# Kernel tuning notes

Measured on AMD Instinct MI355X. Metric: run time of the kernel, lower is better.

## Reference

```python
import jax, jax.numpy as jnp
import numpy as np

N, E, C = 50000, 800000, 100000
D_IN, HID = 128, 128
MLP_IN, MLP_HID = 2 * HID + 1, HID // 2
BN_EPS = 1e-5
NEG_SLOPE = 0.01


def setup_inputs() -> dict:
    key = jax.random.key(0)
    ks = jax.random.split(key, 24)
    inp = {
        "x": jax.random.normal(ks[0], (N, D_IN), jnp.float32),
        "src": jax.random.randint(ks[1], (E,), 0, N, jnp.int32),
        "dst": jax.random.randint(ks[2], (E,), 0, N, jnp.int32),
        "cand_u": jax.random.randint(ks[3], (C,), 0, N, jnp.int32),
        "cand_v": jax.random.randint(ks[4], (C,), 0, N, jnp.int32),
        "cand_feat": jax.random.normal(ks[5], (C, 1), jnp.float32),
    }
    s = 1.0 / np.sqrt(D_IN)
    # SAGEConv layer 0 and 1 (in=out=128 since statedim == pnhid)
    for li, k0 in [(0, 6), (1, 12)]:
        inp[f"w_self{li}"] = jax.random.uniform(ks[k0], (D_IN, HID), jnp.float32, -s, s)
        inp[f"w_neigh{li}"] = jax.random.uniform(ks[k0 + 1], (D_IN, HID), jnp.float32, -s, s)
        inp[f"b{li}"] = jnp.zeros((HID,), jnp.float32)
        inp[f"gamma{li}"] = jnp.ones((HID,), jnp.float32)
        inp[f"beta{li}"] = jnp.zeros((HID,), jnp.float32)
        inp[f"rm{li}"] = jax.random.normal(ks[k0 + 2], (HID,), jnp.float32) * 0.1
        inp[f"rv{li}"] = jax.random.uniform(ks[k0 + 3], (HID,), jnp.float32, 0.5, 1.5)
    # confidence MLP: 257 -> 64 -> 64 -> 1
    sizes = [MLP_IN, MLP_HID, MLP_HID, 1]
    for i in range(3):
        si = 1.0 / np.sqrt(sizes[i])
        inp[f"mw{i}"] = jax.random.uniform(ks[18 + 2 * i], (sizes[i], sizes[i + 1]), jnp.float32, -si, si)
        inp[f"mb{i}"] = jax.random.uniform(ks[19 + 2 * i], (sizes[i + 1],), jnp.float32, -si, si)
    return inp


def _sage_bn_block(x, src, dst, w_self, w_neigh, b, gamma, beta, rm, rv):
    # mean aggregation over incoming edges (gather -> scatter-add -> divide)
    msgs = x[src]  # [E, D]
    agg = jax.ops.segment_sum(msgs, dst, num_segments=N)  # [N, D]
    deg = jax.ops.segment_sum(jnp.ones((src.shape[0],), x.dtype), dst, num_segments=N)
    agg = agg / jnp.maximum(deg, 1.0)[:, None]
    h = x @ w_self + agg @ w_neigh + b
    # BatchNorm1d (eval mode, running stats) then leaky_relu; dropout is identity in eval
    h = gamma * (h - rm) * jax.lax.rsqrt(rv + BN_EPS) + beta
    return jax.nn.leaky_relu(h, NEG_SLOPE)


def reference(x, src, dst, cand_u, cand_v, cand_feat,
              w_self0, w_neigh0, b0, gamma0, beta0, rm0, rv0,
              w_self1, w_neigh1, b1, gamma1, beta1, rm1, rv1,
              mw0, mb0, mw1, mb1, mw2, mb2):
    h = _sage_bn_block(x, src, dst, w_self0, w_neigh0, b0, gamma0, beta0, rm0, rv0)
    h = _sage_bn_block(h, src, dst, w_self1, w_neigh1, b1, gamma1, beta1, rm1, rv1)
    h = jnp.nan_to_num(h, nan=1e-14)
    # candidate embeddings: [C, 2*HID + 1]
    ce = jnp.concatenate([h[cand_u], h[cand_v], cand_feat], axis=-1)
    z = jax.nn.leaky_relu(ce @ mw0 + mb0, NEG_SLOPE)
    z = jax.nn.leaky_relu(z @ mw1 + mb1, NEG_SLOPE)
    y = z @ mw2 + mb2  # [C, 1]
    return y, jax.nn.softmax(y, axis=0)
```

## Files before the change

kernel.cpp:

```cpp
#include <hip/hip_runtime.h>
#include <math.h>

#define N_NODES 50000
#define N_EDGES 800000
#define N_CAND  100000
#define D       128
#define BN_EPS  1e-5f
#define SLOPE   0.01f

#define NB2     196
#define TILE    4096
#define NTILE   196
#define BCAP    4736

typedef __attribute__((ext_vector_type(8))) short bf16x8;
typedef __attribute__((ext_vector_type(4))) float f32x4;

__device__ __forceinline__ float lrelu(float x){ return x >= 0.f ? x : SLOPE * x; }

__device__ __forceinline__ unsigned short f2bf_rn(float f){
  unsigned int u = __float_as_uint(f);
  unsigned int r = u + 0x7FFFu + ((u >> 16) & 1u);
  return (unsigned short)(r >> 16);
}
__device__ __forceinline__ float bf2f(unsigned short h){
  return __uint_as_float(((unsigned int)h) << 16);
}
__device__ __forceinline__ float bfu(unsigned u){ return __uint_as_float(u << 16); }
__device__ __forceinline__ float bfh(unsigned u){ return __uint_as_float(u & 0xffff0000u); }
__device__ __forceinline__ float4 bf4f(ushort4 u){
  return make_float4(__uint_as_float((unsigned)u.x << 16),
                     __uint_as_float((unsigned)u.y << 16),
                     __uint_as_float((unsigned)u.z << 16),
                     __uint_as_float((unsigned)u.w << 16));
}

__device__ __forceinline__ unsigned pk_bf16(float a, float b){
  unsigned r;
  asm("v_cvt_pk_bf16_f32 %0, %1, %2" : "=v"(r) : "v"(a), "v"(b));
  return r;
}
__device__ __forceinline__ void split2(float a, float b, unsigned &h, unsigned &l){
  h = pk_bf16(a, b);
  float ra = a - __uint_as_float(h << 16);
  float rb = b - __uint_as_float(h & 0xffff0000u);
  l = pk_bf16(ra, rb);
}

__global__ __launch_bounds__(256) void k_bin(const int* __restrict__ src, const int* __restrict__ dst,
                                             int* __restrict__ gcnt, unsigned* __restrict__ ebin, int E){
  __shared__ unsigned stage[TILE];
  __shared__ int hist[256], lscan[256], lex[256], lcur[256], gbase[256];
  __shared__ int stot;
  int t = threadIdx.x;
  int e0 = blockIdx.x * TILE;

  hist[t] = 0;
  __syncthreads();

  unsigned pk[16]; int bk[16]; bool ok[16];
  #pragma unroll
  for (int j = 0; j < 16; ++j){
    int i = e0 + j * 256 + t;
    ok[j] = (i < E);
    if (ok[j]){
      int d = dst[i];
      pk[j] = ((unsigned)d << 16) | (unsigned)src[i];
      bk[j] = d >> 8;
      atomicAdd(&hist[bk[j]], 1);
    }
  }
  __syncthreads();

  lscan[t] = hist[t];
  __syncthreads();
  for (int off = 1; off < 256; off <<= 1){
    int v = (t >= off) ? lscan[t - off] : 0;
    __syncthreads();
    lscan[t] += v;
    __syncthreads();
  }
  int ex = lscan[t] - hist[t];
  lex[t]  = ex;
  lcur[t] = ex;
  if (t < NB2) gbase[t] = hist[t] ? atomicAdd(&gcnt[t], hist[t]) : 0;
  if (t == 255) stot = lscan[255];
  __syncthreads();

  #pragma unroll
  for (int j = 0; j < 16; ++j){
    if (ok[j]){
      int p = atomicAdd(&lcur[bk[j]], 1);
      stage[p] = pk[j];
    }
  }
  __syncthreads();

  int tot = stot;
  for (int i = t; i < tot; i += 256){
    unsigned e = stage[i];
    int b = (int)(e >> 24);
    ebin[(size_t)b * BCAP + gbase[b] + (i - lex[b])] = e;
  }
}

__global__ __launch_bounds__(256) void k_bscan2(const int* __restrict__ gcnt, int* __restrict__ bbase,
                                                int* __restrict__ rowptr){
  __shared__ int sd[256];
  int t = threadIdx.x;
  int v = (t < NB2) ? gcnt[t] : 0;
  sd[t] = v; __syncthreads();
  for (int off = 1; off < 256; off <<= 1){
    int a = (t >= off) ? sd[t - off] : 0;
    __syncthreads();
    sd[t] += a; __syncthreads();
  }
  if (t < NB2) bbase[t] = sd[t] - v;
  if (t == NB2 - 1) rowptr[N_NODES] = sd[t];
}

__global__ __launch_bounds__(256) void k_bfin(const int* __restrict__ gcnt, const int* __restrict__ bbase,
                                              const unsigned* __restrict__ ebin,
                                              unsigned short* __restrict__ eid16,
                                              int* __restrict__ rowptr, int n){
  __shared__ int hist[256], lb[256], lcur[256];
  int t = threadIdx.x, b = blockIdx.x;
  int cb   = gcnt[b];
  int base = bbase[b];
  const unsigned* eb = &ebin[(size_t)b * BCAP];
  hist[t] = 0;
  __syncthreads();
  for (int idx = t; idx < cb; idx += 256) atomicAdd(&hist[(eb[idx] >> 16) & 255], 1);
  __syncthreads();
  lb[t] = hist[t];
  __syncthreads();
  for (int off = 1; off < 256; off <<= 1){
    int v = (t >= off) ? lb[t - off] : 0;
    __syncthreads();
    lb[t] += v; __syncthreads();
  }
  int ex = lb[t] - hist[t];
  lcur[t] = ex;
  int node = (b << 8) + t;
  if (node < n) rowptr[node] = base + ex;
  __syncthreads();
  for (int idx = t; idx < cb; idx += 256){
    unsigned e = eb[idx];
    int p = atomicAdd(&lcur[(e >> 16) & 255], 1);
    eid16[base + p] = (unsigned short)(e & 0xffffu);
  }
}

__global__ __launch_bounds__(256) void k_cvt_w(const float* __restrict__ ws, const float* __restrict__ wn,
                                               unsigned short* __restrict__ bth, unsigned short* __restrict__ btl){
  int col = blockIdx.x;
  int k   = threadIdx.x;
  float v = (k < 128) ? ws[k * D + col] : wn[(k - 128) * D + col];
  unsigned short hi = f2bf_rn(v);
  unsigned short lo = f2bf_rn(v - bf2f(hi));
  bth[col * 256 + k] = hi;
  btl[col * 256 + k] = lo;
}

__global__ __launch_bounds__(256) void k_cvt_mlp(const float* __restrict__ w, int K, int Kpad,
                                                 unsigned short* __restrict__ th, unsigned short* __restrict__ tl){
  int col = blockIdx.x;
  for (int k = threadIdx.x; k < Kpad; k += 256){
    float v = (k < K) ? w[k * 64 + col] : 0.f;
    unsigned short hi = f2bf_rn(v);
    th[col * Kpad + k] = hi;
    tl[col * Kpad + k] = f2bf_rn(v - bf2f(hi));
  }
}

__global__ __launch_bounds__(128) void k_cvt_w0cat(const float* __restrict__ mw0,
                                                   unsigned short* __restrict__ ch, unsigned short* __restrict__ cl_){
  int col = blockIdx.x;
  int k   = threadIdx.x;
  float v = (col < 64) ? mw0[k * 64 + col] : mw0[(128 + k) * 64 + (col - 64)];
  unsigned short hi = f2bf_rn(v);
  ch [col * 128 + k] = hi;
  cl_[col * 128 + k] = f2bf_rn(v - bf2f(hi));
}

__global__ __launch_bounds__(256) void k_cvt_x(const float* __restrict__ X, unsigned short* __restrict__ XB, int nel4){
  int i = blockIdx.x * 256 + threadIdx.x;
  if (i < nel4){
    float4 v = *reinterpret_cast<const float4*>(&X[(size_t)i * 4]);
    ushort4 u;
    u.x = f2bf_rn(v.x); u.y = f2bf_rn(v.y); u.z = f2bf_rn(v.z); u.w = f2bf_rn(v.w);
    *reinterpret_cast<ushort4*>(&XB[(size_t)i * 4]) = u;
  }
}

__global__ __launch_bounds__(256) void k_agg_bf(const unsigned short* __restrict__ XB,
                                                const int* __restrict__ rowptr, const unsigned short* __restrict__ eid,
                                                float* __restrict__ AG, int n){
  int g = blockIdx.x * 8 + (threadIdx.x >> 5);
  int l = threadIdx.x & 31;
  if (g >= n) return;
  int e0 = rowptr[g], e1 = rowptr[g + 1];
  float4 a0 = make_float4(0.f,0.f,0.f,0.f);
  float4 a1 = make_float4(0.f,0.f,0.f,0.f);
  float4 a2 = make_float4(0.f,0.f,0.f,0.f);
  float4 a3 = make_float4(0.f,0.f,0.f,0.f);
  int e = e0;
  for (; e + 4 <= e1; e += 4){
    int s0 = eid[e], s1 = eid[e + 1], s2 = eid[e + 2], s3 = eid[e + 3];
    ushort4 u0 = *reinterpret_cast<const ushort4*>(&XB[(size_t)s0 * D + l * 4]);
    ushort4 u1 = *reinterpret_cast<const ushort4*>(&XB[(size_t)s1 * D + l * 4]);
    ushort4 u2 = *reinterpret_cast<const ushort4*>(&XB[(size_t)s2 * D + l * 4]);
    ushort4 u3 = *reinterpret_cast<const ushort4*>(&XB[(size_t)s3 * D + l * 4]);
    float4 f0 = bf4f(u0), f1 = bf4f(u1), f2 = bf4f(u2), f3 = bf4f(u3);
    a0.x += f0.x; a0.y += f0.y; a0.z += f0.z; a0.w += f0.w;
    a1.x += f1.x; a1.y += f1.y; a1.z += f1.z; a1.w += f1.w;
    a2.x += f2.x; a2.y += f2.y; a2.z += f2.z; a2.w += f2.w;
    a3.x += f3.x; a3.y += f3.y; a3.z += f3.z; a3.w += f3.w;
  }
  for (; e < e1; ++e){
    int s0 = eid[e];
    ushort4 u0 = *reinterpret_cast<const ushort4*>(&XB[(size_t)s0 * D + l * 4]);
    float4 f0 = bf4f(u0);
    a0.x += f0.x; a0.y += f0.y; a0.z += f0.z; a0.w += f0.w;
  }
  float sc = 1.f / fmaxf((float)(e1 - e0), 1.f);
  float4 o;
  o.x = (a0.x + a1.x + a2.x + a3.x) * sc;
  o.y = (a0.y + a1.y + a2.y + a3.y) * sc;
  o.z = (a0.z + a1.z + a2.z + a3.z) * sc;
  o.w = (a0.w + a1.w + a2.w + a3.w) * sc;
  *reinterpret_cast<float4*>(&AG[(size_t)g * D + l * 4]) = o;
}

__global__ __launch_bounds__(256) void k_sage_mfma(const float* __restrict__ XS, const float* __restrict__ AG,
    const unsigned short* __restrict__ BTH, const unsigned short* __restrict__ BTL,
    const float* __restrict__ Bb, const float* __restrict__ GM, const float* __restrict__ BT,
    const float* __restrict__ RM, const float* __restrict__ RV,
    float* __restrict__ H, unsigned short* __restrict__ HBH, unsigned short* __restrict__ HBL,
    int n, int donan)
{
  __shared__ unsigned short Ah[64 * 40];
  __shared__ unsigned short Al[64 * 40];
  __shared__ unsigned short Bh[128 * 40];
  __shared__ unsigned short Bl[128 * 40];

  int t  = threadIdx.x;
  int l  = t & 63;
  int wv = t >> 6;
  int lm = l & 15;
  int lk = l >> 4;
  int node0 = blockIdx.x * 64;

  f32x4 acc[8];
  #pragma unroll
  for (int f = 0; f < 8; ++f) acc[f] = (f32x4){0.f, 0.f, 0.f, 0.f};

  for (int step = 0; step < 8; ++step){
    int k0 = step * 32;
    const float* srcA = (step < 4) ? XS : AG;
    int koff = (step < 4) ? k0 : (k0 - 128);

    __syncthreads();
    #pragma unroll
    for (int i = 0; i < 2; ++i){
      int c   = t + i * 256;
      int row = c >> 3, c4 = c & 7;
      int node = min(node0 + row, n - 1);
      float4 v = *reinterpret_cast<const float4*>(&srcA[(size_t)node * D + koff + c4 * 4]);
      const float* vp = (const float*)&v;
      unsigned short hh[4], ll[4];
      #pragma unroll
      for (int j = 0; j < 4; ++j){
        unsigned short hi = f2bf_rn(vp[j]);
        hh[j] = hi;
        ll[j] = f2bf_rn(vp[j] - bf2f(hi));
      }
      uint2 wh, wl;
      wh.x = (unsigned)hh[0] | ((unsigned)hh[1] << 16);
      wh.y = (unsigned)hh[2] | ((unsigned)hh[3] << 16);
      wl.x = (unsigned)ll[0] | ((unsigned)ll[1] << 16);
      wl.y = (unsigned)ll[2] | ((unsigned)ll[3] << 16);
      *reinterpret_cast<uint2*>(&Ah[row * 40 + c4 * 4]) = wh;
      *reinterpret_cast<uint2*>(&Al[row * 40 + c4 * 4]) = wl;
    }
    #pragma unroll
    for (int i = 0; i < 2; ++i){
      int c   = t + i * 256;
      int col = c >> 2, q = c & 3;
      *reinterpret_cast<uint4*>(&Bh[col * 40 + q * 8]) =
          *reinterpret_cast<const uint4*>(&BTH[col * 256 + k0 + q * 8]);
      *reinterpret_cast<uint4*>(&Bl[col * 40 + q * 8]) =
          *reinterpret_cast<const uint4*>(&BTL[col * 256 + k0 + q * 8]);
    }
    __syncthreads();

    bf16x8 afh = *reinterpret_cast<const bf16x8*>(&Ah[(wv * 16 + lm) * 40 + lk * 8]);
    bf16x8 afl = *reinterpret_cast<const bf16x8*>(&Al[(wv * 16 + lm) * 40 + lk * 8]);
    #pragma unroll
    for (int f = 0; f < 8; ++f){
      bf16x8 bfh = *reinterpret_cast<const bf16x8*>(&Bh[(f * 16 + lm) * 40 + lk * 8]);
      bf16x8 bfl = *reinterpret_cast<const bf16x8*>(&Bl[(f * 16 + lm) * 40 + lk * 8]);
      acc[f] = __builtin_amdgcn_mfma_f32_16x16x32_bf16(afh, bfh, acc[f], 0, 0, 0);
      acc[f] = __builtin_amdgcn_mfma_f32_16x16x32_bf16(afl, bfh, acc[f], 0, 0, 0);
      acc[f] = __builtin_amdgcn_mfma_f32_16x16x32_bf16(afh, bfl, acc[f], 0, 0, 0);
    }
  }

  #pragma unroll
  for (int f = 0; f < 8; ++f){
    int col = f * 16 + lm;
    float s  = GM[col] * rsqrtf(RV[col] + BN_EPS);
    float cj = (Bb[col] - RM[col]) * s + BT[col];
    #pragma unroll
    for (int r = 0; r < 4; ++r){
      int node = node0 + wv * 16 + lk * 4 + r;
      if (node < n){
        float v = lrelu(acc[f][r] * s + cj);
        if (donan && (v != v)) v = 1e-14f;
        if (H)  H[(size_t)node * D + col] = v;
        unsigned short h16 = f2bf_rn(v);
        if (HBH) HBH[(size_t)node * D + col] = h16;
        if (HBL) HBL[(size_t)node * D + col] = f2bf_rn(v - bf2f(h16));
      }
    }
  }
}

__global__ __launch_bounds__(256) void k_pgemm(
    const unsigned short* __restrict__ HH, const unsigned short* __restrict__ HL,
    const unsigned short* __restrict__ WCH, const unsigned short* __restrict__ WCL,
    unsigned short* __restrict__ PH, unsigned short* __restrict__ PL, int n)
{
  __shared__ unsigned short Ah[64 * 40];
  __shared__ unsigned short Al[64 * 40];
  __shared__ unsigned short Bh[128 * 40];
  __shared__ unsigned short Bl[128 * 40];

  int t  = threadIdx.x;
  int l  = t & 63;
  int wv = t >> 6;
  int lm = l & 15;
  int lk = l >> 4;
  int node0 = blockIdx.x * 64;

  f32x4 acc[8];
  #pragma unroll
  for (int f = 0; f < 8; ++f) acc[f] = (f32x4){0.f, 0.f, 0.f, 0.f};

  for (int step = 0; step < 4; ++step){
    int k0 = step * 32;
    __syncthreads();
    {
      int row = t >> 2, q = t & 3;
      int node = min(node0 + row, n - 1);
      *reinterpret_cast<uint4*>(&Ah[row * 40 + q * 8]) =
          *reinterpret_cast<const uint4*>(&HH[(size_t)node * D + k0 + q * 8]);
      *reinterpret_cast<uint4*>(&Al[row * 40 + q * 8]) =
          *reinterpret_cast<const uint4*>(&HL[(size_t)node * D + k0 + q * 8]);
    }
    #pragma unroll
    for (int i = 0; i < 2; ++i){
      int c = t + i * 256;
      int col = c >> 2, q = c & 3;
      *reinterpret_cast<uint4*>(&Bh[col * 40 + q * 8]) =
          *reinterpret_cast<const uint4*>(&WCH[col * 128 + k0 + q * 8]);
      *reinterpret_cast<uint4*>(&Bl[col * 40 + q * 8]) =
          *reinterpret_cast<const uint4*>(&WCL[col * 128 + k0 + q * 8]);
    }
    __syncthreads();

    bf16x8 afh = *reinterpret_cast<const bf16x8*>(&Ah[(wv * 16 + lm) * 40 + lk * 8]);
    bf16x8 afl = *reinterpret_cast<const bf16x8*>(&Al[(wv * 16 + lm) * 40 + lk * 8]);
    #pragma unroll
    for (int f = 0; f < 8; ++f){
      bf16x8 bfh = *reinterpret_cast<const bf16x8*>(&Bh[(f * 16 + lm) * 40 + lk * 8]);
      bf16x8 bfl = *reinterpret_cast<const bf16x8*>(&Bl[(f * 16 + lm) * 40 + lk * 8]);
      acc[f] = __builtin_amdgcn_mfma_f32_16x16x32_bf16(afh, bfh, acc[f], 0, 0, 0);
      acc[f] = __builtin_amdgcn_mfma_f32_16x16x32_bf16(afl, bfh, acc[f], 0, 0, 0);
      acc[f] = __builtin_amdgcn_mfma_f32_16x16x32_bf16(afh, bfl, acc[f], 0, 0, 0);
    }
  }

  #pragma unroll
  for (int f = 0; f < 8; ++f){
    int col = f * 16 + lm;
    #pragma unroll
    for (int r = 0; r < 4; ++r){
      int node = node0 + wv * 16 + lk * 4 + r;
      if (node < n){
        float v = acc[f][r];
        unsigned short h16 = f2bf_rn(v);
        PH[(size_t)node * D + col] = h16;
        PL[(size_t)node * D + col] = f2bf_rn(v - bf2f(h16));
      }
    }
  }
}

__device__ __forceinline__ void proc2(unsigned uh, unsigned ul, unsigned vh, unsigned vl,
                                      float wfa, float wfb, float b0a, float b0b, float cfv,
                                      unsigned &ho, unsigned &lo_){
  float z0 = lrelu(bfu(uh) + bfu(ul) + bfu(vh) + bfu(vl) + cfv * wfa + b0a);
  float z1 = lrelu(bfh(uh) + bfh(ul) + bfh(vh) + bfh(vl) + cfv * wfb + b0b);
  split2(z0, z1, ho, lo_);
}

__global__ __launch_bounds__(256) void k_mlp2(
    const unsigned short* __restrict__ PH, const unsigned short* __restrict__ PL,
    const int* __restrict__ cu, const int* __restrict__ cv, const float* __restrict__ cf,
    const float* __restrict__ mw0, const float* __restrict__ mb0,
    const unsigned short* __restrict__ W1H, const unsigned short* __restrict__ W1L,
    const float* __restrict__ mb1, const float* __restrict__ mw2, const float* __restrict__ mb2,
    float* __restrict__ y, int C)
{
  __shared__ unsigned short zh[4][32 * 72];
  __shared__ unsigned short zl[4][32 * 72];
  __shared__ float bw[64], ww[64];

  int t = threadIdx.x;
  int wv = t >> 6, l = t & 63, lm = l & 15, lk = l >> 4;
  int cl = l & 31, hsel = l >> 5;
  int candbase = blockIdx.x * 128 + wv * 32;

  if (t < 64){ bw[t] = mb0[t]; ww[t] = mw0[256 * 64 + t]; }
  __syncthreads();

  int cc = min(candbase + cl, C - 1);
  int nu = cu[cc], nv = cv[cc];
  float cfv = cf[cc];

  const uint4* puh = reinterpret_cast<const uint4*>(&PH[(size_t)nu * D + hsel * 32]);
  const uint4* pul = reinterpret_cast<const uint4*>(&PL[(size_t)nu * D + hsel * 32]);
  const uint4* pvh = reinterpret_cast<const uint4*>(&PH[(size_t)nv * D + 64 + hsel * 32]);
  const uint4* pvl = reinterpret_cast<const uint4*>(&PL[(size_t)nv * D + 64 + hsel * 32]);
  uint4 uh0 = puh[0], uh1 = puh[1], uh2 = puh[2], uh3 = puh[3];
  uint4 ul0 = pul[0], ul1 = pul[1], ul2 = pul[2], ul3 = pul[3];
  uint4 vh0 = pvh[0], vh1 = pvh[1], vh2 = pvh[2], vh3 = pvh[3];
  uint4 vl0 = pvl[0], vl1 = pvl[1], vl2 = pvl[2], vl3 = pvl[3];

  int colb = hsel * 32;
  unsigned short* zhr = &zh[wv][cl * 72];
  unsigned short* zlr = &zl[wv][cl * 72];
  #define PROC_W(UH, UL, VH, VL, CO) { \
    unsigned ho, lo_; \
    proc2(UH, UL, VH, VL, ww[colb + (CO)], ww[colb + (CO) + 1], bw[colb + (CO)], bw[colb + (CO) + 1], cfv, ho, lo_); \
    *reinterpret_cast<unsigned*>(&zhr[colb + (CO)]) = ho; \
    *reinterpret_cast<unsigned*>(&zlr[colb + (CO)]) = lo_; }
  PROC_W(uh0.x, ul0.x, vh0.x, vl0.x, 0)  PROC_W(uh0.y, ul0.y, vh0.y, vl0.y, 2)
  PROC_W(uh0.z, ul0.z, vh0.z, vl0.z, 4)  PROC_W(uh0.w, ul0.w, vh0.w, vl0.w, 6)
  PROC_W(uh1.x, ul1.x, vh1.x, vl1.x, 8)  PROC_W(uh1.y, ul1.y, vh1.y, vl1.y, 10)
  PROC_W(uh1.z, ul1.z, vh1.z, vl1.z, 12) PROC_W(uh1.w, ul1.w, vh1.w, vl1.w, 14)
  PROC_W(uh2.x, ul2.x, vh2.x, vl2.x, 16) PROC_W(uh2.y, ul2.y, vh2.y, vl2.y, 18)
  PROC_W(uh2.z, ul2.z, vh2.z, vl2.z, 20) PROC_W(uh2.w, ul2.w, vh2.w, vl2.w, 22)
  PROC_W(uh3.x, ul3.x, vh3.x, vl3.x, 24) PROC_W(uh3.y, ul3.y, vh3.y, vl3.y, 26)
  PROC_W(uh3.z, ul3.z, vh3.z, vl3.z, 28) PROC_W(uh3.w, ul3.w, vh3.w, vl3.w, 30)
  #undef PROC_W

  int kbase = lk * 8;
  f32x4 a2[2][4];
  #pragma unroll
  for (int m = 0; m < 2; ++m)
    #pragma unroll
    for (int f = 0; f < 4; ++f) a2[m][f] = (f32x4){0.f, 0.f, 0.f, 0.f};

  #pragma unroll
  for (int s2 = 0; s2 < 2; ++s2){
    int kk = s2 * 32 + kbase;
    bf16x8 azh0 = *reinterpret_cast<const bf16x8*>(&zh[wv][(0 * 16 + lm) * 72 + kk]);
    bf16x8 azl0 = *reinterpret_cast<const bf16x8*>(&zl[wv][(0 * 16 + lm) * 72 + kk]);
    bf16x8 azh1 = *reinterpret_cast<const bf16x8*>(&zh[wv][(1 * 16 + lm) * 72 + kk]);
    bf16x8 azl1 = *reinterpret_cast<const bf16x8*>(&zl[wv][(1 * 16 + lm) * 72 + kk]);
    #pragma unroll
    for (int f = 0; f < 4; ++f){
      int col = f * 16 + lm;
      bf16x8 bh = *reinterpret_cast<const bf16x8*>(&W1H[(size_t)col * 64 + kk]);
      bf16x8 bl = *reinterpret_cast<const bf16x8*>(&W1L[(size_t)col * 64 + kk]);
      a2[0][f] = __builtin_amdgcn_mfma_f32_16x16x32_bf16(azh0, bh, a2[0][f], 0, 0, 0);
      a2[0][f] = __builtin_amdgcn_mfma_f32_16x16x32_bf16(azl0, bh, a2[0][f], 0, 0, 0);
      a2[0][f] = __builtin_amdgcn_mfma_f32_16x16x32_bf16(azh0, bl, a2[0][f], 0, 0, 0);
      a2[1][f] = __builtin_amdgcn_mfma_f32_16x16x32_bf16(azh1, bh, a2[1][f], 0, 0, 0);
      a2[1][f] = __builtin_amdgcn_mfma_f32_16x16x32_bf16(azl1, bh, a2[1][f], 0, 0, 0);
      a2[1][f] = __builtin_amdgcn_mfma_f32_16x16x32_bf16(azh1, bl, a2[1][f], 0, 0, 0);
    }
  }

  float p00 = 0.f, p01 = 0.f, p02 = 0.f, p03 = 0.f;
  float p10 = 0.f, p11 = 0.f, p12 = 0.f, p13 = 0.f;
  #pragma unroll
  for (int f = 0; f < 4; ++f){
    int col = f * 16 + lm;
    float b1v = mb1[col];
    float w2v = mw2[col];
    p00 = fmaf(lrelu(a2[0][f][0] + b1v), w2v, p00);
    p01 = fmaf(lrelu(a2[0][f][1] + b1v), w2v, p01);
    p02 = fmaf(lrelu(a2[0][f][2] + b1v), w2v, p02);
    p03 = fmaf(lrelu(a2[0][f][3] + b1v), w2v, p03);
    p10 = fmaf(lrelu(a2[1][f][0] + b1v), w2v, p10);
    p11 = fmaf(lrelu(a2[1][f][1] + b1v), w2v, p11);
    p12 = fmaf(lrelu(a2[1][f][2] + b1v), w2v, p12);
    p13 = fmaf(lrelu(a2[1][f][3] + b1v), w2v, p13);
  }
  #pragma unroll
  for (int off = 1; off < 16; off <<= 1){
    p00 += __shfl_xor(p00, off); p01 += __shfl_xor(p01, off);
    p02 += __shfl_xor(p02, off); p03 += __shfl_xor(p03, off);
    p10 += __shfl_xor(p10, off); p11 += __shfl_xor(p11, off);
    p12 += __shfl_xor(p12, off); p13 += __shfl_xor(p13, off);
  }
  if (lm == 0){
    float b2 = mb2[0];
    int base0 = candbase + lk * 4;
    int base1 = candbase + 16 + lk * 4;
    if (base0 + 0 < C) y[base0 + 0] = p00 + b2;
    if (base0 + 1 < C) y[base0 + 1] = p01 + b2;
    if (base0 + 2 < C) y[base0 + 2] = p02 + b2;
    if (base0 + 3 < C) y[base0 + 3] = p03 + b2;
    if (base1 + 0 < C) y[base1 + 0] = p10 + b2;
    if (base1 + 1 < C) y[base1 + 1] = p11 + b2;
    if (base1 + 2 < C) y[base1 + 2] = p12 + b2;
    if (base1 + 3 < C) y[base1 + 3] = p13 + b2;
  }
}

__global__ __launch_bounds__(256) void k_red1(const float* __restrict__ y,
                                              float* __restrict__ bmax, float* __restrict__ bsum, int C){
  __shared__ float sm[4];
  __shared__ float ss[4];
  int t = threadIdx.x;
  float m = -3.4e38f;
  for (int i = blockIdx.x * 256 + t; i < C; i += gridDim.x * 256) m = fmaxf(m, y[i]);
  for (int o = 32; o; o >>= 1) m = fmaxf(m, __shfl_xor(m, o));
  if ((t & 63) == 0) sm[t >> 6] = m;
  __syncthreads();
  float bm = fmaxf(fmaxf(sm[0], sm[1]), fmaxf(sm[2], sm[3]));
  float s = 0.f;
  for (int i = blockIdx.x * 256 + t; i < C; i += gridDim.x * 256) s += expf(y[i] - bm);
  for (int o = 32; o; o >>= 1) s += __shfl_xor(s, o);
  if ((t & 63) == 0) ss[t >> 6] = s;
  __syncthreads();
  if (t == 0){ bmax[blockIdx.x] = bm; bsum[blockIdx.x] = ss[0] + ss[1] + ss[2] + ss[3]; }
}

__global__ __launch_bounds__(256) void k_red2(const float* __restrict__ bmax, const float* __restrict__ bsum,
                                              float* __restrict__ g, int nb){
  __shared__ float sm[4];
  __shared__ float ss[4];
  int t = threadIdx.x;
  float m0 = (t < nb) ? bmax[t] : -3.4e38f;
  float m = m0;
  for (int o = 32; o; o >>= 1) m = fmaxf(m, __shfl_xor(m, o));
  if ((t & 63) == 0) sm[t >> 6] = m;
  __syncthreads();
  float gm = fmaxf(fmaxf(sm[0], sm[1]), fmaxf(sm[2], sm[3]));
  float s = (t < nb) ? bsum[t] * expf(m0 - gm) : 0.f;
  for (int o = 32; o; o >>= 1) s += __shfl_xor(s, o);
  if ((t & 63) == 0) ss[t >> 6] = s;
  __syncthreads();
  if (t == 0){ g[0] = gm; g[1] = 1.f / (ss[0] + ss[1] + ss[2] + ss[3]); }
}

__global__ __launch_bounds__(256) void k_red3(const float* __restrict__ y, const float* __restrict__ g,
                                              float* __restrict__ out, int C){
  int i = blockIdx.x * 256 + threadIdx.x;
  if (i < C) out[i] = expf(y[i] - g[0]) * g[1];
}

extern "C" void kernel_launch(void* const* d_in, const int* in_sizes, int n_in,
                              void* d_out, int out_size, void* d_ws, size_t ws_size,
                              hipStream_t stream)
{
  const float* x   = (const float*)d_in[0];
  const int*   src = (const int*)  d_in[1];
  const int*   dst = (const int*)  d_in[2];
  const int*   cu  = (const int*)  d_in[3];
  const int*   cv  = (const int*)  d_in[4];
  const float* cf  = (const float*)d_in[5];
  const float* ws0 = (const float*)d_in[6];
  const float* wn0 = (const float*)d_in[7];
  const float* b0  = (const float*)d_in[8];
  const float* g0  = (const float*)d_in[9];
  const float* be0 = (const float*)d_in[10];
  const float* rm0 = (const float*)d_in[11];
  const float* rv0 = (const float*)d_in[12];
  const float* ws1 = (const float*)d_in[13];
  const float* wn1 = (const float*)d_in[14];
  const float* b1  = (const float*)d_in[15];
  const float* g1  = (const float*)d_in[16];
  const float* be1 = (const float*)d_in[17];
  const float* rm1 = (const float*)d_in[18];
  const float* rv1 = (const float*)d_in[19];
  const float* mw0 = (const float*)d_in[20];
  const float* mb0 = (const float*)d_in[21];
  const float* mw1 = (const float*)d_in[22];
  const float* mb1 = (const float*)d_in[23];
  const float* mw2 = (const float*)d_in[24];
  const float* mb2 = (const float*)d_in[25];

  float* out = (float*)d_out;

  char* w = (char*)d_ws;
  float* aggn  = (float*)w; w += (size_t)N_NODES * D * 4;
  float* h0    = (float*)w; w += (size_t)N_NODES * D * 4;
  float* h1    = (float*)w; w += (size_t)N_NODES * D * 4;
  int* cnt     = (int*)w;   w += (size_t)N_NODES * 4;
  int* rowptr  = (int*)w;   w += (size_t)(N_NODES + 1) * 4;
  int* cur     = (int*)w;   w += (size_t)N_NODES * 4;
  int* eid     = (int*)w;   w += (size_t)N_EDGES * 4;
  int* gcnt    = (int*)w;   w += (size_t)(NB2 + 8) * 4;
  int* bbase   = (int*)w;   w += (size_t)(NB2 + 1) * 4;
  float* bmax  = (float*)w; w += 256 * 4;
  float* bsumF = (float*)w; w += 256 * 4;
  float* gred  = (float*)w; w += 2 * 4;
  unsigned short* w1th  = (unsigned short*)w; w += (size_t)64 * 64 * 2;
  unsigned short* w1tl  = (unsigned short*)w; w += (size_t)64 * 64 * 2;
  unsigned short* w0cth = (unsigned short*)w; w += (size_t)128 * 128 * 2;
  unsigned short* w0ctl = (unsigned short*)w; w += (size_t)128 * 128 * 2;

  unsigned short* eid16 = (unsigned short*)eid;

  unsigned* ebin = (unsigned*)h0;

  unsigned short* xb   = (unsigned short*)h1;
  unsigned short* hb0  = xb + (size_t)N_NODES * D;
  unsigned short* hb1h = (unsigned short*)h1;
  unsigned short* hb1l = hb1h + (size_t)N_NODES * D;

  unsigned short* pbh = (unsigned short*)aggn;
  unsigned short* pbl = pbh + (size_t)N_NODES * D;

  unsigned short* bth0 = (unsigned short*)cnt;
  unsigned short* btl0 = bth0 + 128 * 256;
  unsigned short* bth1 = (unsigned short*)cur;
  unsigned short* btl1 = bth1 + 128 * 256;

  hipMemsetAsync(gcnt, 0, (size_t)NB2 * 4, stream);
  k_bin   <<<NTILE, 256, 0, stream>>>(src, dst, gcnt, ebin, N_EDGES);
  k_bscan2<<<1, 256, 0, stream>>>(gcnt, bbase, rowptr);
  k_bfin  <<<NB2, 256, 0, stream>>>(gcnt, bbase, ebin, eid16, rowptr, N_NODES);

  k_cvt_w<<<128, 256, 0, stream>>>(ws0, wn0, bth0, btl0);
  k_cvt_w<<<128, 256, 0, stream>>>(ws1, wn1, bth1, btl1);
  k_cvt_mlp<<<64, 256, 0, stream>>>(mw1, 64, 64, w1th, w1tl);
  k_cvt_w0cat<<<128, 128, 0, stream>>>(mw0, w0cth, w0ctl);
  k_cvt_x<<<(N_NODES * D / 4 + 255) / 256, 256, 0, stream>>>(x, xb, N_NODES * D / 4);

  int GB = (N_NODES + 63) / 64;
  k_agg_bf<<<(N_NODES + 7) / 8, 256, 0, stream>>>(xb, rowptr, eid16, aggn, N_NODES);
  k_sage_mfma<<<GB, 256, 0, stream>>>(x,  aggn, bth0, btl0, b0, g0, be0, rm0, rv0,
                                      h0, hb0, (unsigned short*)0, N_NODES, 0);
  k_agg_bf<<<(N_NODES + 7) / 8, 256, 0, stream>>>(hb0, rowptr, eid16, aggn, N_NODES);
  k_sage_mfma<<<GB, 256, 0, stream>>>(h0, aggn, bth1, btl1, b1, g1, be1, rm1, rv1,
                                      (float*)0, hb1h, hb1l, N_NODES, 1);

  k_pgemm<<<GB, 256, 0, stream>>>(hb1h, hb1l, w0cth, w0ctl, pbh, pbl, N_NODES);

  k_mlp2<<<(N_CAND + 127) / 128, 256, 0, stream>>>(pbh, pbl, cu, cv, cf,
      mw0, mb0, w1th, w1tl, mb1, mw2, mb2, out, N_CAND);

  k_red1<<<256, 256, 0, stream>>>(out, bmax, bsumF, N_CAND);
  k_red2<<<1, 256, 0, stream>>>(bmax, bsumF, gred, 256);
  k_red3<<<(N_CAND + 255) / 256, 256, 0, stream>>>(out, gred, out + N_CAND, N_CAND);
}
```

Measured before the change: 227.6 us.

## Store activations as bf16 hi/lo pairs and merge weight/input prep kernels

The fp32 activations and aggregation buffers become pre-split bf16 hi/lo arrays, written by the producers (the prep kernel, the aggregation kernel and the SAGE epilogue). The GEMM then loads them straight into shared memory instead of converting fp32 on every tile load. The fp32 h0 output is dropped, and five small conversion launches are folded into one k_prep kernel. Memory traffic stays about the same, since hi plus lo equals fp32 size, but the repeated split arithmetic moves out of the GEMM and fewer launches are issued. The change relies on a split2 helper that the visible diff does not define.

```diff
diff --git a/kernel.cpp b/kernel.cpp
--- a/kernel.cpp
+++ b/kernel.cpp
@@ -151,51 +151,64 @@
   }
 }
 
-__global__ __launch_bounds__(256) void k_cvt_w(const float* __restrict__ ws, const float* __restrict__ wn,
-                                               unsigned short* __restrict__ bth, unsigned short* __restrict__ btl){
-  int col = blockIdx.x;
-  int k   = threadIdx.x;
-  float v = (k < 128) ? ws[k * D + col] : wn[(k - 128) * D + col];
-  unsigned short hi = f2bf_rn(v);
-  unsigned short lo = f2bf_rn(v - bf2f(hi));
-  bth[col * 256 + k] = hi;
-  btl[col * 256 + k] = lo;
-}
-
-__global__ __launch_bounds__(256) void k_cvt_mlp(const float* __restrict__ w, int K, int Kpad,
-                                                 unsigned short* __restrict__ th, unsigned short* __restrict__ tl){
-  int col = blockIdx.x;
-  for (int k = threadIdx.x; k < Kpad; k += 256){
-    float v = (k < K) ? w[k * 64 + col] : 0.f;
+__global__ __launch_bounds__(256) void k_prep(
+    const float* __restrict__ ws0, const float* __restrict__ wn0,
+    const float* __restrict__ ws1, const float* __restrict__ wn1,
+    const float* __restrict__ mw0, const float* __restrict__ mw1,
+    const float* __restrict__ X,
+    unsigned short* __restrict__ bth0, unsigned short* __restrict__ btl0,
+    unsigned short* __restrict__ bth1, unsigned short* __restrict__ btl1,
+    unsigned short* __restrict__ w1th, unsigned short* __restrict__ w1tl,
+    unsigned short* __restrict__ w0cth, unsigned short* __restrict__ w0ctl,
+    unsigned short* __restrict__ XH, unsigned short* __restrict__ XL)
+{
+  int b = blockIdx.x, t = threadIdx.x;
+  if (b < 256){
+    int col = b & 127;
+    const float* wsp = (b < 128) ? ws0 : ws1;
+    const float* wnp = (b < 128) ? wn0 : wn1;
+    unsigned short* th = (b < 128) ? bth0 : bth1;
+    unsigned short* tl = (b < 128) ? btl0 : btl1;
+    float v = (t < 128) ? wsp[t * D + col] : wnp[(t - 128) * D + col];
     unsigned short hi = f2bf_rn(v);
-    th[col * Kpad + k] = hi;
-    tl[col * Kpad + k] = f2bf_rn(v - bf2f(hi));
-  }
-}
-
-__global__ __launch_bounds__(128) void k_cvt_w0cat(const float* __restrict__ mw0,
-                                                   unsigned short* __restrict__ ch, unsigned short* __restrict__ cl_){
-  int col = blockIdx.x;
-  int k   = threadIdx.x;
-  float v = (col < 64) ? mw0[k * 64 + col] : mw0[(128 + k) * 64 + (col - 64)];
-  unsigned short hi = f2bf_rn(v);
-  ch [col * 128 + k] = hi;
-  cl_[col * 128 + k] = f2bf_rn(v - bf2f(hi));
-}
-
-__global__ __launch_bounds__(256) void k_cvt_x(const float* __restrict__ X, unsigned short* __restrict__ XB, int nel4){
-  int i = blockIdx.x * 256 + threadIdx.x;
-  if (i < nel4){
-    float4 v = *reinterpret_cast<const float4*>(&X[(size_t)i * 4]);
-    ushort4 u;
-    u.x = f2bf_rn(v.x); u.y = f2bf_rn(v.y); u.z = f2bf_rn(v.z); u.w = f2bf_rn(v.w);
-    *reinterpret_cast<ushort4*>(&XB[(size_t)i * 4]) = u;
+    th[col * 256 + t] = hi;
+    tl[col * 256 + t] = f2bf_rn(v - bf2f(hi));
+  } else if (b < 320){
+    if (t < 64){
+      int col = b - 256;
+      float v = mw1[t * 64 + col];
+      unsigned short hi = f2bf_rn(v);
+      w1th[col * 64 + t] = hi;
+      w1tl[col * 64 + t] = f2bf_rn(v - bf2f(hi));
+    }
+  } else if (b < 448){
+    if (t < 128){
+      int col = b - 320;
+      float v = (col < 64) ? mw0[t * 64 + col] : mw0[(128 + t) * 64 + (col - 64)];
+      unsigned short hi = f2bf_rn(v);
+      w0cth[col * 128 + t] = hi;
+      w0ctl[col * 128 + t] = f2bf_rn(v - bf2f(hi));
+    }
+  } else {
+    int i = (b - 448) * 256 + t;
+    if (i < N_NODES * D / 8){
+      const float4* xp = reinterpret_cast<const float4*>(&X[(size_t)i * 8]);
+      float4 v0 = xp[0], v1 = xp[1];
+      uint4 h, l;
+      split2(v0.x, v0.y, h.x, l.x);
+      split2(v0.z, v0.w, h.y, l.y);
+      split2(v1.x, v1.y, h.z, l.z);
+      split2(v1.z, v1.w, h.w, l.w);
+      *reinterpret_cast<uint4*>(&XH[(size_t)i * 8]) = h;
+      *reinterpret_cast<uint4*>(&XL[(size_t)i * 8]) = l;
+    }
   }
 }
 
 __global__ __launch_bounds__(256) void k_agg_bf(const unsigned short* __restrict__ XB,
                                                 const int* __restrict__ rowptr, const unsigned short* __restrict__ eid,
-                                                float* __restrict__ AG, int n){
+                                                unsigned short* __restrict__ AGH, unsigned short* __restrict__ AGL,
+                                                int n){
   int g = blockIdx.x * 8 + (threadIdx.x >> 5);
   int l = threadIdx.x & 31;
   if (g >= n) return;
@@ -224,19 +237,24 @@
     a0.x += f0.x; a0.y += f0.y; a0.z += f0.z; a0.w += f0.w;
   }
   float sc = 1.f / fmaxf((float)(e1 - e0), 1.f);
-  float4 o;
-  o.x = (a0.x + a1.x + a2.x + a3.x) * sc;
-  o.y = (a0.y + a1.y + a2.y + a3.y) * sc;
-  o.z = (a0.z + a1.z + a2.z + a3.z) * sc;
-  o.w = (a0.w + a1.w + a2.w + a3.w) * sc;
-  *reinterpret_cast<float4*>(&AG[(size_t)g * D + l * 4]) = o;
-}
-
-__global__ __launch_bounds__(256) void k_sage_mfma(const float* __restrict__ XS, const float* __restrict__ AG,
+  float ox = (a0.x + a1.x + a2.x + a3.x) * sc;
+  float oy = (a0.y + a1.y + a2.y + a3.y) * sc;
+  float oz = (a0.z + a1.z + a2.z + a3.z) * sc;
+  float ow = (a0.w + a1.w + a2.w + a3.w) * sc;
+  uint2 h, lo_;
+  split2(ox, oy, h.x, lo_.x);
+  split2(oz, ow, h.y, lo_.y);
+  *reinterpret_cast<uint2*>(&AGH[(size_t)g * D + l * 4]) = h;
+  *reinterpret_cast<uint2*>(&AGL[(size_t)g * D + l * 4]) = lo_;
+}
+
+__global__ __launch_bounds__(256) void k_sage_mfma(
+    const unsigned short* __restrict__ A0H, const unsigned short* __restrict__ A0L,
+    const unsigned short* __restrict__ A1H, const unsigned short* __restrict__ A1L,
     const unsigned short* __restrict__ BTH, const unsigned short* __restrict__ BTL,
     const float* __restrict__ Bb, const float* __restrict__ GM, const float* __restrict__ BT,
     const float* __restrict__ RM, const float* __restrict__ RV,
-    float* __restrict__ H, unsigned short* __restrict__ HBH, unsigned short* __restrict__ HBL,
+    unsigned short* __restrict__ HBH, unsigned short* __restrict__ HBL,
     int n, int donan)
 {
   __shared__ unsigned short Ah[64 * 40];
@@ -257,31 +275,18 @@
 
   for (int step = 0; step < 8; ++step){
     int k0 = step * 32;
-    const float* srcA = (step < 4) ? XS : AG;
+    const unsigned short* srcH = (step < 4) ? A0H : A1H;
+    const unsigned short* srcL = (step < 4) ? A0L : A1L;
     int koff = (step < 4) ? k0 : (k0 - 128);
 
     __syncthreads();
-    #pragma unroll
-    for (int i = 0; i < 2; ++i){
-      int c   = t + i * 256;
-      int row = c >> 3, c4 = c & 7;
+    {
+      int row = t >> 2, q = t & 3;
       int node = min(node0 + row, n - 1);
-      float4 v = *reinterpret_cast<const float4*>(&srcA[(size_t)node * D + koff + c4 * 4]);
-      const float* vp = (const float*)&v;
-      unsigned short hh[4], ll[4];
-      #pragma unroll
-      for (int j = 0; j < 4; ++j){
-        unsigned short hi = f2bf_rn(vp[j]);
-        hh[j] = hi;
-        ll[j] = f2bf_rn(vp[j] - bf2f(hi));
-      }
-      uint2 wh, wl;
-      wh.x = (unsigned)hh[0] | ((unsigned)hh[1] << 16);
-      wh.y = (unsigned)hh[2] | ((unsigned)hh[3] << 16);
-      wl.x = (unsigned)ll[0] | ((unsigned)ll[1] << 16);
-      wl.y = (unsigned)ll[2] | ((unsigned)ll[3] << 16);
-      *reinterpret_cast<uint2*>(&Ah[row * 40 + c4 * 4]) = wh;
-      *reinterpret_cast<uint2*>(&Al[row * 40 + c4 * 4]) = wl;
+      *reinterpret_cast<uint4*>(&Ah[row * 40 + q * 8]) =
+          *reinterpret_cast<const uint4*>(&srcH[(size_t)node * D + koff + q * 8]);
+      *reinterpret_cast<uint4*>(&Al[row * 40 + q * 8]) =
+          *reinterpret_cast<const uint4*>(&srcL[(size_t)node * D + koff + q * 8]);
     }
     #pragma unroll
     for (int i = 0; i < 2; ++i){
@@ -317,10 +322,9 @@
       if (node < n){
         float v = lrelu(acc[f][r] * s + cj);
         if (donan && (v != v)) v = 1e-14f;
-        if (H)  H[(size_t)node * D + col] = v;
         unsigned short h16 = f2bf_rn(v);
-        if (HBH) HBH[(size_t)node * D + col] = h16;
-        if (HBL) HBL[(size_t)node * D + col] = f2bf_rn(v - bf2f(h16));
+        HBH[(size_t)node * D + col] = h16;
+        HBL[(size_t)node * D + col] = f2bf_rn(v - bf2f(h16));
       }
     }
   }
@@ -599,9 +603,9 @@
   float* out = (float*)d_out;
 
   char* w = (char*)d_ws;
-  float* aggn  = (float*)w; w += (size_t)N_NODES * D * 4;
-  float* h0    = (float*)w; w += (size_t)N_NODES * D * 4;
-  float* h1    = (float*)w; w += (size_t)N_NODES * D * 4;
+  char* regA = w; w += (size_t)N_NODES * D * 4;
+  char* regB = w; w += (size_t)N_NODES * D * 4;
+  char* regC = w; w += (size_t)N_NODES * D * 4;
   int* cnt     = (int*)w;   w += (size_t)N_NODES * 4;
   int* rowptr  = (int*)w;   w += (size_t)(N_NODES + 1) * 4;
   int* cur     = (int*)w;   w += (size_t)N_NODES * 4;
@@ -618,14 +622,16 @@
 
   unsigned short* eid16 = (unsigned short*)eid;
 
-  unsigned* ebin = (unsigned*)h0;
-
-  unsigned short* xb   = (unsigned short*)h1;
-  unsigned short* hb0  = xb + (size_t)N_NODES * D;
-  unsigned short* hb1h = (unsigned short*)h1;
+  unsigned* ebin = (unsigned*)regB;
+  unsigned short* hb0h = (unsigned short*)regB;
+  unsigned short* hb0l = hb0h + (size_t)N_NODES * D;
+  unsigned short* xh   = (unsigned short*)regC;
+  unsigned short* xl   = xh + (size_t)N_NODES * D;
+  unsigned short* hb1h = (unsigned short*)regC;
   unsigned short* hb1l = hb1h + (size_t)N_NODES * D;
-
-  unsigned short* pbh = (unsigned short*)aggn;
+  unsigned short* agh = (unsigned short*)regA;
+  unsigned short* agl = agh + (size_t)N_NODES * D;
+  unsigned short* pbh = (unsigned short*)regA;
   unsigned short* pbl = pbh + (size_t)N_NODES * D;
 
   unsigned short* bth0 = (unsigned short*)cnt;
@@ -638,19 +644,17 @@
   k_bscan2<<<1, 256, 0, stream>>>(gcnt, bbase, rowptr);
   k_bfin  <<<NB2, 256, 0, stream>>>(gcnt, bbase, ebin, eid16, rowptr, N_NODES);
 
-  k_cvt_w<<<128, 256, 0, stream>>>(ws0, wn0, bth0, btl0);
-  k_cvt_w<<<128, 256, 0, stream>>>(ws1, wn1, bth1, btl1);
-  k_cvt_mlp<<<64, 256, 0, stream>>>(mw1, 64, 64, w1th, w1tl);
-  k_cvt_w0cat<<<128, 128, 0, stream>>>(mw0, w0cth, w0ctl);
-  k_cvt_x<<<(N_NODES * D / 4 + 255) / 256, 256, 0, stream>>>(x, xb, N_NODES * D / 4);
+  int PREPB = 448 + (N_NODES * D / 8 + 255) / 256;
+  k_prep<<<PREPB, 256, 0, stream>>>(ws0, wn0, ws1, wn1, mw0, mw1, x,
+      bth0, btl0, bth1, btl1, w1th, w1tl, w0cth, w0ctl, xh, xl);
 
   int GB = (N_NODES + 63) / 64;
-  k_agg_bf<<<(N_NODES + 7) / 8, 256, 0, stream>>>(xb, rowptr, eid16, aggn, N_NODES);
-  k_sage_mfma<<<GB, 256, 0, stream>>>(x,  aggn, bth0, btl0, b0, g0, be0, rm0, rv0,
-                                      h0, hb0, (unsigned short*)0, N_NODES, 0);
-  k_agg_bf<<<(N_NODES + 7) / 8, 256, 0, stream>>>(hb0, rowptr, eid16, aggn, N_NODES);
-  k_sage_mfma<<<GB, 256, 0, stream>>>(h0, aggn, bth1, btl1, b1, g1, be1, rm1, rv1,
-                                      (float*)0, hb1h, hb1l, N_NODES, 1);
+  k_agg_bf<<<(N_NODES + 7) / 8, 256, 0, stream>>>(xh, rowptr, eid16, agh, agl, N_NODES);
+  k_sage_mfma<<<GB, 256, 0, stream>>>(xh, xl, agh, agl, bth0, btl0,
+                                      b0, g0, be0, rm0, rv0, hb0h, hb0l, N_NODES, 0);
+  k_agg_bf<<<(N_NODES + 7) / 8, 256, 0, stream>>>(hb0h, rowptr, eid16, agh, agl, N_NODES);
+  k_sage_mfma<<<GB, 256, 0, stream>>>(hb0h, hb0l, agh, agl, bth1, btl1,
+                                      b1, g1, be1, rm1, rv1, hb1h, hb1l, N_NODES, 1);
 
   k_pgemm<<<GB, 256, 0, stream>>>(hb1h, hb1l, w0cth, w0ctl, pbh, pbl, N_NODES);
 
```

Result: faster. 210.1 us (median of 2 runs) (-7.7%).
